# Optimization experiments

Hardware: AMD Instinct MI355X
Metric: run time of the kernel (lower is better)

## Reference

```python
import jax, jax.numpy as jnp
import numpy as np


def _fps(xyz, npoint):
    # Farthest point sampling. xyz: [B, N, 3] -> indices [B, npoint] (int32)
    B, N, _ = xyz.shape
    def step(carry, _):
        dist, far = carry
        centroid = jnp.take_along_axis(xyz, far[:, None, None], axis=1)  # [B,1,3]
        d = jnp.sum((xyz - centroid) ** 2, axis=-1)                      # [B,N]
        dist = jnp.minimum(dist, d)
        nxt = jnp.argmax(dist, axis=-1).astype(jnp.int32)
        return (dist, nxt), far
    init = (jnp.full((B, N), 1e10, xyz.dtype), jnp.zeros((B,), jnp.int32))
    _, inds = jax.lax.scan(step, init, None, length=npoint)
    return jnp.transpose(inds)  # [B, npoint]


def _gather(x, idx):
    # x: [B, N, C]; idx: [B, ...] -> [B, ..., C]
    return jax.vmap(lambda xb, ib: xb[ib])(x, idx)


def _knn(query, ref, k):
    # query: [B, M, 3]; ref: [B, N, 3] -> neighbor idx [B, M, k]
    d = (jnp.sum(query ** 2, -1, keepdims=True)
         - 2.0 * jnp.einsum('bmc,bnc->bmn', query, ref)
         + jnp.sum(ref ** 2, -1)[:, None, :])
    _, idx = jax.lax.top_k(-d, k)
    return idx


def _set_conv(xyz, feat, npoint, k, Ws, bs):
    # FPS downsample + KNN group + shared MLP + max-pool (FlowNet3D-style SetConv)
    fidx = _fps(xyz, npoint)
    new_xyz = _gather(xyz, fidx)                       # [B, npoint, 3]
    nidx = _knn(new_xyz, xyz, k)                       # [B, npoint, k]
    h = jnp.concatenate([_gather(xyz, nidx) - new_xyz[:, :, None, :],
                         _gather(feat, nidx)], axis=-1)
    for W, b in zip(Ws, bs):
        h = jax.nn.relu(h @ W + b)
    return jnp.max(h, axis=2), new_xyz, fidx


def _set_up_conv(cx, fx, cf, ff, k, Ws1, bs1, Ws2, bs2):
    # KNN from fine points into coarse set + MLP + max-pool + skip-concat + MLP
    nidx = _knn(fx, cx, k)                             # [B, M_fine, k]
    h = jnp.concatenate([_gather(cx, nidx) - fx[:, :, None, :],
                         _gather(cf, nidx)], axis=-1)
    for W, b in zip(Ws1, bs1):
        h = jax.nn.relu(h @ W + b)
    h = jnp.concatenate([jnp.max(h, axis=2), ff], axis=-1)
    for W, b in zip(Ws2, bs2):
        h = jax.nn.relu(h @ W + b)
    return h


def setup_inputs() -> dict:
    key = jax.random.key(0)
    ks = iter(jax.random.split(key, 64))
    def w(shape):
        return jax.random.normal(next(ks), shape, jnp.float32) / np.float32(np.sqrt(shape[0]))
    def z(n):
        return jnp.zeros((n,), jnp.float32)
    inp = {
        'pc': jax.random.normal(next(ks), (2, 8192, 3), jnp.float32),
        'feat': jax.random.normal(next(ks), (2, 8192, 3), jnp.float32),
        'd0_W': w((3, 32)), 'd0_b': z(32),
        'd1_W0': w((35, 32)), 'd1_b0': z(32), 'd1_W1': w((32, 64)), 'd1_b1': z(64),
        'd2_W0': w((67, 64)), 'd2_b0': z(64), 'd2_W1': w((64, 128)), 'd2_b1': z(128),
        'd3_W0': w((131, 128)), 'd3_b0': z(128), 'd3_W1': w((128, 192)), 'd3_b1': z(192),
        'd4_W0': w((195, 192)), 'd4_b0': z(192), 'd4_W1': w((192, 192)), 'd4_b1': z(192),
        'u4_W1': w((195, 192)), 'u4_b1': z(192), 'u4_W2': w((384, 192)), 'u4_b2': z(192),
        'u3_W1': w((195, 128)), 'u3_b1': z(128), 'u3_W2': w((256, 128)), 'u3_b2': z(128),
        'u2_W1': w((131, 64)), 'u2_b1': z(64), 'u2_W2': w((128, 64)), 'u2_b2': z(64),
        'u1_W1': w((67, 32)), 'u1_b1': z(32), 'u1_W2': w((64, 32)), 'u1_b2': z(32),
    }
    return inp


def reference(pc, feat,
              d0_W, d0_b,
              d1_W0, d1_b0, d1_W1, d1_b1,
              d2_W0, d2_b0, d2_W1, d2_b1,
              d3_W0, d3_b0, d3_W1, d3_b1,
              d4_W0, d4_b0, d4_W1, d4_b1,
              u4_W1, u4_b1, u4_W2, u4_b2,
              u3_W1, u3_b1, u3_W2, u3_b2,
              u2_W1, u2_b1, u2_W2, u2_b2,
              u1_W1, u1_b1, u1_W2, u1_b2):
    # gts[0] is None branch of GenFlow_unit_mask.forward: pure encoder pyramid.
    f0 = jax.nn.relu(feat @ d0_W + d0_b)                                   # down0 (1x1 Conv1d)
    f1, x1, i1 = _set_conv(pc, f0, 2048, 16, [d1_W0, d1_W1], [d1_b0, d1_b1])
    f2, x2, i2 = _set_conv(x1, f1, 512, 16, [d2_W0, d2_W1], [d2_b0, d2_b1])
    f3, x3, i3 = _set_conv(x2, f2, 128, 16, [d3_W0, d3_W1], [d3_b0, d3_b1])
    f4, x4, i4 = _set_conv(x3, f3, 64, 16, [d4_W0, d4_W1], [d4_b0, d4_b1])
    u3 = _set_up_conv(x4, x3, f4, f3, 8, [u4_W1], [u4_b1], [u4_W2], [u4_b2])
    u2 = _set_up_conv(x3, x2, u3, f2, 8, [u3_W1], [u3_b1], [u3_W2], [u3_b2])
    u1 = _set_up_conv(x2, x1, u2, f1, 8, [u2_W1], [u2_b1], [u2_W2], [u2_b2])
    u0 = _set_up_conv(x1, pc, u1, f0, 8, [u1_W1], [u1_b1], [u1_W2], [u1_b2])
    return (x1, x2, x3, i1, i2, i3, u0, u1, u2, u3)
```

## Files before the change

kernel.cpp:

```cpp
#include <hip/hip_runtime.h>
#include <cstdint>
#include <cstddef>


static __device__ __forceinline__ float sq3_rn(float x, float y, float z) {
    return __fadd_rn(__fadd_rn(__fmul_rn(x, x), __fmul_rn(y, y)), __fmul_rn(z, z));
}

static __device__ __forceinline__ unsigned int ford(float f) {
    unsigned int u = __float_as_uint(f);
    return u ^ ((u >> 31) ? 0xFFFFFFFFu : 0x80000000u);
}

template <int CTRL>
static __device__ __forceinline__ void dpp_max_step(unsigned& hi, unsigned& lo) {
    unsigned h2 = (unsigned)__builtin_amdgcn_update_dpp((int)hi, (int)hi, CTRL, 0xf, 0xf, false);
    unsigned l2 = (unsigned)__builtin_amdgcn_update_dpp((int)lo, (int)lo, CTRL, 0xf, 0xf, false);
    if (h2 > hi || (h2 == hi && l2 > lo)) { hi = h2; lo = l2; }
}
template <int CTRL>
static __device__ __forceinline__ void dpp_min_step(unsigned& hi, unsigned& lo) {
    unsigned h2 = (unsigned)__builtin_amdgcn_update_dpp((int)hi, (int)hi, CTRL, 0xf, 0xf, false);
    unsigned l2 = (unsigned)__builtin_amdgcn_update_dpp((int)lo, (int)lo, CTRL, 0xf, 0xf, false);
    if (h2 < hi || (h2 == hi && l2 < lo)) { hi = h2; lo = l2; }
}
static __device__ __forceinline__ void dpp_reduce_max_u64(unsigned& hi, unsigned& lo) {
    dpp_max_step<0x111>(hi, lo);
    dpp_max_step<0x112>(hi, lo);
    dpp_max_step<0x114>(hi, lo);
    dpp_max_step<0x118>(hi, lo);
    dpp_max_step<0x142>(hi, lo);
    dpp_max_step<0x143>(hi, lo);
}
static __device__ __forceinline__ void dpp_reduce_min_u64(unsigned& hi, unsigned& lo) {
    dpp_min_step<0x111>(hi, lo);
    dpp_min_step<0x112>(hi, lo);
    dpp_min_step<0x114>(hi, lo);
    dpp_min_step<0x118>(hi, lo);
    dpp_min_step<0x142>(hi, lo);
    dpp_min_step<0x143>(hi, lo);
}
static __device__ __forceinline__ void dpp_reduce_max_u64_4(unsigned& hi, unsigned& lo) {
    dpp_max_step<0x111>(hi, lo);
    dpp_max_step<0x112>(hi, lo);
}

template <int T, int P, bool MIRROR>
__global__ __launch_bounds__(T)
__attribute__((amdgpu_waves_per_eu(1, 1), amdgpu_num_vgpr(256)))
void fps_block(const float* __restrict__ xyz, int M,
               float* __restrict__ new_xyz, float* __restrict__ out_idx)
{
    constexpr int N = T * P;
    constexpr int NW = T / 64;
    static_assert(NW == 4, "slot scan hardcoded for 4 waves");
    const int b = blockIdx.x;
    const int t = threadIdx.x;
    const int lane = t & 63, wave = t >> 6;

    __shared__ unsigned long long s_slot[2][NW];
    __shared__ float spts[MIRROR ? N * 3 : 1];

    const float* x0 = xyz + (size_t)b * N * 3;
    if (MIRROR) {
        for (int i = t; i < N * 3; i += T) spts[i] = x0[i];
    }

    float px[P], py[P], pz[P], dist[P];
#pragma unroll
    for (int j = 0; j < P; ++j) {
        int p = j * T + t;
        px[j] = x0[p * 3 + 0];
        py[j] = x0[p * 3 + 1];
        pz[j] = x0[p * 3 + 2];
        dist[j] = 1e10f;
    }
    if (MIRROR) __syncthreads();

    int far = 0;
    for (int m = 0; m < M; ++m) {
        float cx, cy, cz;
        if (MIRROR) {
            cx = spts[far * 3 + 0];
            cy = spts[far * 3 + 1];
            cz = spts[far * 3 + 2];
        } else {
            cx = x0[far * 3 + 0];
            cy = x0[far * 3 + 1];
            cz = x0[far * 3 + 2];
        }
        if (t == 0) {
            size_t o = (size_t)b * M + m;
            new_xyz[o * 3 + 0] = cx;
            new_xyz[o * 3 + 1] = cy;
            new_xyz[o * 3 + 2] = cz;
            if (out_idx) out_idx[o] = (float)far;
        }
        float bv = -1.0f;
        int   bj = 0;
#pragma unroll
        for (int j = 0; j < P; ++j) {
            float dx = __fsub_rn(px[j], cx);
            float dy = __fsub_rn(py[j], cy);
            float dz = __fsub_rn(pz[j], cz);
            float d  = sq3_rn(dx, dy, dz);
            float nd = fminf(dist[j], d);
            dist[j] = nd;
            if (nd > bv) { bv = nd; bj = j; }
        }
        int bp = bj * T + t;
        unsigned hi = __float_as_uint(bv);
        unsigned lo = 0x7fffffffu - (unsigned)bp;
        dpp_reduce_max_u64(hi, lo);
        if (lane == 63)
            s_slot[m & 1][wave] = ((unsigned long long)hi << 32) | lo;
        __syncthreads();
        unsigned long long sv = s_slot[m & 1][lane & 3];
        unsigned shi = (unsigned)(sv >> 32), slo = (unsigned)(sv & 0xffffffffu);
        dpp_reduce_max_u64_4(shi, slo);
        unsigned wlo = (unsigned)__builtin_amdgcn_readlane((int)slo, 63);
        far = 0x7fffffff - (int)wlo;
    }
}

template <int P>
__global__ __launch_bounds__(64) __attribute__((amdgpu_waves_per_eu(1, 1)))
void fps_wave(const float* __restrict__ xyz, int M,
              float* __restrict__ new_xyz, float* __restrict__ out_idx)
{
    const int b = blockIdx.x;
    const int lane = threadIdx.x;
    const int N = 64 * P;
    const float* x0 = xyz + (size_t)b * N * 3;

    float px[P], py[P], pz[P], dist[P];
#pragma unroll
    for (int j = 0; j < P; ++j) {
        int p = j * 64 + lane;
        px[j] = x0[p * 3 + 0];
        py[j] = x0[p * 3 + 1];
        pz[j] = x0[p * 3 + 2];
        dist[j] = 1e10f;
    }

    int far = 0;
    for (int m = 0; m < M; ++m) {
        float cx = x0[far * 3 + 0];
        float cy = x0[far * 3 + 1];
        float cz = x0[far * 3 + 2];
        if (lane == 0) {
            size_t o = (size_t)b * M + m;
            new_xyz[o * 3 + 0] = cx;
            new_xyz[o * 3 + 1] = cy;
            new_xyz[o * 3 + 2] = cz;
            if (out_idx) out_idx[o] = (float)far;
        }
        float bv = -1.0f;
        int   bj = 0;
#pragma unroll
        for (int j = 0; j < P; ++j) {
            float dx = __fsub_rn(px[j], cx);
            float dy = __fsub_rn(py[j], cy);
            float dz = __fsub_rn(pz[j], cz);
            float d  = sq3_rn(dx, dy, dz);
            float nd = fminf(dist[j], d);
            dist[j] = nd;
            if (nd > bv) { bv = nd; bj = j; }
        }
        int bp = bj * 64 + lane;
        unsigned hi = __float_as_uint(bv);
        unsigned lo = 0x7fffffffu - (unsigned)bp;
        dpp_reduce_max_u64(hi, lo);
        unsigned wlo = (unsigned)__builtin_amdgcn_readlane((int)lo, 63);
        far = 0x7fffffff - (int)wlo;
    }
}

#define KNN_QPB 4
template <int K>
__global__ void knn_wave(const float* __restrict__ query, int M,
                         const float* __restrict__ ref, int N,
                         int* __restrict__ nidx)
{
    const int b = blockIdx.y;
    const int m = blockIdx.x * KNN_QPB + threadIdx.y;
    const int lane = threadIdx.x;
    if (m >= M) return;

    const float* qp = query + ((size_t)b * M + m) * 3;
    const float qx = qp[0], qy = qp[1], qz = qp[2];
    const float sq = sq3_rn(qx, qy, qz);

    float dk[K];
    int   ik[K];
#pragma unroll
    for (int j = 0; j < K; ++j) { dk[j] = INFINITY; ik[j] = 0x7fffffff; }

    const float* rb = ref + (size_t)b * N * 3;
    for (int n = lane; n < N; n += 64) {
        const float* rp = rb + (size_t)n * 3;
        float rx = rp[0], ry = rp[1], rz = rp[2];
        float sr = sq3_rn(rx, ry, rz);
        float dot = __fadd_rn(__fadd_rn(__fmul_rn(qx, rx), __fmul_rn(qy, ry)),
                              __fmul_rn(qz, rz));
        float d = __fadd_rn(__fsub_rn(sq, __fmul_rn(2.0f, dot)), sr);
        if (d < dk[K - 1]) {
            dk[K - 1] = d;
            ik[K - 1] = n;
#pragma unroll
            for (int j = K - 1; j > 0; --j) {
                if (dk[j] < dk[j - 1]) {
                    float tv = dk[j]; dk[j] = dk[j - 1]; dk[j - 1] = tv;
                    int   ti = ik[j]; ik[j] = ik[j - 1]; ik[j - 1] = ti;
                }
            }
        }
    }

    unsigned long long arr[K];
#pragma unroll
    for (int j = 0; j < K; ++j)
        arr[j] = ((unsigned long long)ford(dk[j]) << 32) | (unsigned int)ik[j];

    int winner = 0;
    for (int r = 0; r < K; ++r) {
        unsigned hi = (unsigned)(arr[0] >> 32);
        unsigned lo = (unsigned)(arr[0] & 0xffffffffu);
        dpp_reduce_min_u64(hi, lo);
        unsigned bhi = (unsigned)__builtin_amdgcn_readlane((int)hi, 63);
        unsigned blo = (unsigned)__builtin_amdgcn_readlane((int)lo, 63);
        unsigned long long best = ((unsigned long long)bhi << 32) | blo;
        if (lane == r) winner = (int)blo;
        if (arr[0] == best) {
#pragma unroll
            for (int j = 0; j < K - 1; ++j) arr[j] = arr[j + 1];
            arr[K - 1] = ~0ull;
        }
    }
    int* op = nidx + ((size_t)b * M + m) * K;
    if (lane < K) op[lane] = winner;
}

template <int K>
__global__ void setconv_kernel(const float* __restrict__ ref_xyz, int N,
                               const float* __restrict__ ref_feat, int Cin,
                               const float* __restrict__ new_xyz, int M,
                               const int* __restrict__ nidx,
                               const float* __restrict__ W0, const float* __restrict__ b0, int C1,
                               const float* __restrict__ W1, const float* __restrict__ b1, int C2,
                               float* __restrict__ out)
{
    const int b = blockIdx.y, q = blockIdx.x;
    const int lane = threadIdx.x;
    const int Cin3 = Cin + 3;
    extern __shared__ float sm[];
    float* h  = sm;
    float* h1 = sm + K * Cin3;

    const size_t qg = (size_t)b * M + q;
    const float cx = new_xyz[qg * 3 + 0];
    const float cy = new_xyz[qg * 3 + 1];
    const float cz = new_xyz[qg * 3 + 2];

    int nj[K];
#pragma unroll
    for (int j = 0; j < K; ++j) nj[j] = nidx[qg * K + j];

#pragma unroll
    for (int j = 0; j < K; ++j) {
        const float* xp = ref_xyz + ((size_t)b * N + nj[j]) * 3;
        const float* fp = ref_feat + ((size_t)b * N + nj[j]) * Cin;
        for (int i = lane; i < Cin3; i += 64) {
            float v;
            if (i == 0)      v = __fsub_rn(xp[0], cx);
            else if (i == 1) v = __fsub_rn(xp[1], cy);
            else if (i == 2) v = __fsub_rn(xp[2], cz);
            else             v = fp[i - 3];
            h[j * Cin3 + i] = v;
        }
    }
    __syncthreads();

    for (int c0 = 0; c0 < C1; c0 += 64) {
        int c = c0 + lane;
        bool act = c < C1;
        float acc[K];
        float bias = act ? b0[c] : 0.0f;
#pragma unroll
        for (int j = 0; j < K; ++j) acc[j] = bias;
        for (int i = 0; i < Cin3; ++i) {
            float w = act ? W0[(size_t)i * C1 + c] : 0.0f;
#pragma unroll
            for (int j = 0; j < K; ++j) acc[j] = fmaf(h[j * Cin3 + i], w, acc[j]);
        }
        if (act) {
#pragma unroll
            for (int j = 0; j < K; ++j) h1[j * C1 + c] = fmaxf(acc[j], 0.0f);
        }
    }
    __syncthreads();

    for (int c0 = 0; c0 < C2; c0 += 64) {
        int c = c0 + lane;
        bool act = c < C2;
        float acc[K];
        float bias = act ? b1[c] : 0.0f;
#pragma unroll
        for (int j = 0; j < K; ++j) acc[j] = bias;
        for (int i = 0; i < C1; ++i) {
            float w = act ? W1[(size_t)i * C2 + c] : 0.0f;
#pragma unroll
            for (int j = 0; j < K; ++j) acc[j] = fmaf(h1[j * C1 + i], w, acc[j]);
        }
        if (act) {
            float mv = acc[0];
#pragma unroll
            for (int j = 1; j < K; ++j) mv = fmaxf(mv, acc[j]);
            out[qg * C2 + c] = fmaxf(mv, 0.0f);
        }
    }
}

template <int K>
__global__ void setupconv_kernel(const float* __restrict__ cxyz, int Nc,
                                 const float* __restrict__ cf, int Cc,
                                 const float* __restrict__ fxyz, int M,
                                 const float* __restrict__ ff, int Cf,
                                 const int* __restrict__ nidx,
                                 const float* __restrict__ W1, const float* __restrict__ b1, int C1,
                                 const float* __restrict__ W2, const float* __restrict__ b2, int C2,
                                 float* __restrict__ out)
{
    const int b = blockIdx.y, q = blockIdx.x;
    const int lane = threadIdx.x;
    const int Cc3 = Cc + 3;
    extern __shared__ float sm[];
    float* h = sm;
    float* g = sm + K * Cc3;

    const size_t qg = (size_t)b * M + q;
    const float px = fxyz[qg * 3 + 0];
    const float py = fxyz[qg * 3 + 1];
    const float pz = fxyz[qg * 3 + 2];

    int nj[K];
#pragma unroll
    for (int j = 0; j < K; ++j) nj[j] = nidx[qg * K + j];

#pragma unroll
    for (int j = 0; j < K; ++j) {
        const float* xp = cxyz + ((size_t)b * Nc + nj[j]) * 3;
        const float* fp = cf + ((size_t)b * Nc + nj[j]) * Cc;
        for (int i = lane; i < Cc3; i += 64) {
            float v;
            if (i == 0)      v = __fsub_rn(xp[0], px);
            else if (i == 1) v = __fsub_rn(xp[1], py);
            else if (i == 2) v = __fsub_rn(xp[2], pz);
            else             v = fp[i - 3];
            h[j * Cc3 + i] = v;
        }
    }
    for (int i = lane; i < Cf; i += 64) g[C1 + i] = ff[qg * Cf + i];
    __syncthreads();

    for (int c0 = 0; c0 < C1; c0 += 64) {
        int c = c0 + lane;
        bool act = c < C1;
        float acc[K];
        float bias = act ? b1[c] : 0.0f;
#pragma unroll
        for (int j = 0; j < K; ++j) acc[j] = bias;
        for (int i = 0; i < Cc3; ++i) {
            float w = act ? W1[(size_t)i * C1 + c] : 0.0f;
#pragma unroll
            for (int j = 0; j < K; ++j) acc[j] = fmaf(h[j * Cc3 + i], w, acc[j]);
        }
        if (act) {
            float mv = acc[0];
#pragma unroll
            for (int j = 1; j < K; ++j) mv = fmaxf(mv, acc[j]);
            g[c] = fmaxf(mv, 0.0f);
        }
    }
    __syncthreads();

    const int Cg = C1 + Cf;
    for (int c0 = 0; c0 < C2; c0 += 64) {
        int c = c0 + lane;
        bool act = c < C2;
        float acc = act ? b2[c] : 0.0f;
        for (int i = 0; i < Cg; ++i) {
            float w = act ? W2[(size_t)i * C2 + c] : 0.0f;
            acc = fmaf(g[i], w, acc);
        }
        if (act) out[qg * C2 + c] = fmaxf(acc, 0.0f);
    }
}

__global__ void f0_kernel(const float* __restrict__ feat, const float* __restrict__ W,
                          const float* __restrict__ bias, float* __restrict__ out)
{
    int t = blockIdx.x * blockDim.x + threadIdx.x;
    int n = t >> 5, c = t & 31;
    const float* f = feat + (size_t)n * 3;
    float acc = bias[c];
    acc = fmaf(f[0], W[c], acc);
    acc = fmaf(f[1], W[32 + c], acc);
    acc = fmaf(f[2], W[64 + c], acc);
    out[t] = fmaxf(acc, 0.0f);
}


extern "C" void kernel_launch(void* const* d_in, const int* in_sizes, int n_in,
                              void* d_out, int out_size, void* d_ws, size_t ws_size,
                              hipStream_t stream)
{
    const float* pc    = (const float*)d_in[0];
    const float* feat  = (const float*)d_in[1];
    const float* d0_W  = (const float*)d_in[2];
    const float* d0_b  = (const float*)d_in[3];
    const float* d1_W0 = (const float*)d_in[4];
    const float* d1_b0 = (const float*)d_in[5];
    const float* d1_W1 = (const float*)d_in[6];
    const float* d1_b1 = (const float*)d_in[7];
    const float* d2_W0 = (const float*)d_in[8];
    const float* d2_b0 = (const float*)d_in[9];
    const float* d2_W1 = (const float*)d_in[10];
    const float* d2_b1 = (const float*)d_in[11];
    const float* d3_W0 = (const float*)d_in[12];
    const float* d3_b0 = (const float*)d_in[13];
    const float* d3_W1 = (const float*)d_in[14];
    const float* d3_b1 = (const float*)d_in[15];
    const float* d4_W0 = (const float*)d_in[16];
    const float* d4_b0 = (const float*)d_in[17];
    const float* d4_W1 = (const float*)d_in[18];
    const float* d4_b1 = (const float*)d_in[19];
    const float* u4_W1 = (const float*)d_in[20];
    const float* u4_b1 = (const float*)d_in[21];
    const float* u4_W2 = (const float*)d_in[22];
    const float* u4_b2 = (const float*)d_in[23];
    const float* u3_W1 = (const float*)d_in[24];
    const float* u3_b1 = (const float*)d_in[25];
    const float* u3_W2 = (const float*)d_in[26];
    const float* u3_b2 = (const float*)d_in[27];
    const float* u2_W1 = (const float*)d_in[28];
    const float* u2_b1 = (const float*)d_in[29];
    const float* u2_W2 = (const float*)d_in[30];
    const float* u2_b2 = (const float*)d_in[31];
    const float* u1_W1 = (const float*)d_in[32];
    const float* u1_b1 = (const float*)d_in[33];
    const float* u1_W2 = (const float*)d_in[34];
    const float* u1_b2 = (const float*)d_in[35];

    float* out = (float*)d_out;
    float* o_x1 = out + 0;
    float* o_x2 = out + 12288;
    float* o_x3 = out + 15360;
    float* o_i1 = out + 16128;
    float* o_i2 = out + 20224;
    float* o_i3 = out + 21248;
    float* o_u0 = out + 21504;
    float* o_u1 = out + 545792;
    float* o_u2 = out + 807936;
    float* o_u3 = out + 939008;

    float* w = (float*)d_ws;
    float* f0 = w; w += 2 * 8192 * 32;
    float* f1 = w; w += 2 * 2048 * 64;
    float* f2 = w; w += 2 * 512 * 128;
    float* f3 = w; w += 2 * 128 * 192;
    float* f4 = w; w += 2 * 64 * 192;
    float* x4 = w; w += 2 * 64 * 3;
    int* nidx = (int*)w;

    const int B = 2;
    const dim3 kb(64, KNN_QPB);

    f0_kernel<<<(2 * 8192 * 32) / 256, 256, 0, stream>>>(feat, d0_W, d0_b, f0);

    fps_block<256, 32, false><<<B, 256, 0, stream>>>(pc, 2048, o_x1, o_i1);
    knn_wave<16><<<dim3(2048 / KNN_QPB, B), kb, 0, stream>>>(o_x1, 2048, pc, 8192, nidx);
    setconv_kernel<16><<<dim3(2048, B), 64, (16 * 35 + 16 * 32) * 4, stream>>>(
        pc, 8192, f0, 32, o_x1, 2048, nidx, d1_W0, d1_b0, 32, d1_W1, d1_b1, 64, f1);

    fps_block<256, 8, true><<<B, 256, 0, stream>>>(o_x1, 512, o_x2, o_i2);
    knn_wave<16><<<dim3(512 / KNN_QPB, B), kb, 0, stream>>>(o_x2, 512, o_x1, 2048, nidx);
    setconv_kernel<16><<<dim3(512, B), 64, (16 * 67 + 16 * 64) * 4, stream>>>(
        o_x1, 2048, f1, 64, o_x2, 512, nidx, d2_W0, d2_b0, 64, d2_W1, d2_b1, 128, f2);

    fps_wave<8><<<B, 64, 0, stream>>>(o_x2, 128, o_x3, o_i3);
    knn_wave<16><<<dim3(128 / KNN_QPB, B), kb, 0, stream>>>(o_x3, 128, o_x2, 512, nidx);
    setconv_kernel<16><<<dim3(128, B), 64, (16 * 131 + 16 * 128) * 4, stream>>>(
        o_x2, 512, f2, 128, o_x3, 128, nidx, d3_W0, d3_b0, 128, d3_W1, d3_b1, 192, f3);

    fps_wave<2><<<B, 64, 0, stream>>>(o_x3, 64, x4, nullptr);
    knn_wave<16><<<dim3(64 / KNN_QPB, B), kb, 0, stream>>>(x4, 64, o_x3, 128, nidx);
    setconv_kernel<16><<<dim3(64, B), 64, (16 * 195 + 16 * 192) * 4, stream>>>(
        o_x3, 128, f3, 192, x4, 64, nidx, d4_W0, d4_b0, 192, d4_W1, d4_b1, 192, f4);

    knn_wave<8><<<dim3(128 / KNN_QPB, B), kb, 0, stream>>>(o_x3, 128, x4, 64, nidx);
    setupconv_kernel<8><<<dim3(128, B), 64, (8 * 195 + 192 + 192) * 4, stream>>>(
        x4, 64, f4, 192, o_x3, 128, f3, 192, nidx,
        u4_W1, u4_b1, 192, u4_W2, u4_b2, 192, o_u3);

    knn_wave<8><<<dim3(512 / KNN_QPB, B), kb, 0, stream>>>(o_x2, 512, o_x3, 128, nidx);
    setupconv_kernel<8><<<dim3(512, B), 64, (8 * 195 + 128 + 128) * 4, stream>>>(
        o_x3, 128, o_u3, 192, o_x2, 512, f2, 128, nidx,
        u3_W1, u3_b1, 128, u3_W2, u3_b2, 128, o_u2);

    knn_wave<8><<<dim3(2048 / KNN_QPB, B), kb, 0, stream>>>(o_x1, 2048, o_x2, 512, nidx);
    setupconv_kernel<8><<<dim3(2048, B), 64, (8 * 131 + 64 + 64) * 4, stream>>>(
        o_x2, 512, o_u2, 128, o_x1, 2048, f1, 64, nidx,
        u2_W1, u2_b1, 64, u2_W2, u2_b2, 64, o_u1);

    knn_wave<8><<<dim3(8192 / KNN_QPB, B), kb, 0, stream>>>(pc, 8192, o_x1, 2048, nidx);
    setupconv_kernel<8><<<dim3(8192, B), 64, (8 * 67 + 32 + 32) * 4, stream>>>(
        o_x1, 2048, o_u1, 64, pc, 8192, f0, 32, nidx,
        u1_W1, u1_b1, 32, u1_W2, u1_b2, 32, o_u0);
}
```

Before: 4.259 ms.

## Move FPS x/y coordinates to LDS and simplify cross-wave argmax

Farthest-point-sampling blocks now keep only z and running distances in registers, storing x/y pairs for all but the last slot in dynamically sized LDS. This cuts register pressure (the forced 256-VGPR attribute is dropped) at the cost of an LDS read per point on every iteration. The LDS point mirror is removed, so centroids are read from global memory each step. The cross-wave reduction is now a scalar loop over wave slots instead of a DPP reduction plus readlane.

```diff
diff --git a/kernel.cpp b/kernel.cpp
--- a/kernel.cpp
+++ b/kernel.cpp
@@ -40,55 +40,43 @@
     dpp_min_step<0x142>(hi, lo);
     dpp_min_step<0x143>(hi, lo);
 }
-static __device__ __forceinline__ void dpp_reduce_max_u64_4(unsigned& hi, unsigned& lo) {
-    dpp_max_step<0x111>(hi, lo);
-    dpp_max_step<0x112>(hi, lo);
-}
-
-template <int T, int P, bool MIRROR>
-__global__ __launch_bounds__(T)
-__attribute__((amdgpu_waves_per_eu(1, 1), amdgpu_num_vgpr(256)))
+
+template <int T, int P>
+__global__ __launch_bounds__(T) __attribute__((amdgpu_waves_per_eu(1, 1)))
 void fps_block(const float* __restrict__ xyz, int M,
                float* __restrict__ new_xyz, float* __restrict__ out_idx)
 {
     constexpr int N = T * P;
     constexpr int NW = T / 64;
-    static_assert(NW == 4, "slot scan hardcoded for 4 waves");
+    constexpr int NL = N - T;
+    extern __shared__ char smem[];
+    float2* sxy = (float2*)smem;
+    unsigned long long* s_slot = (unsigned long long*)(smem + (size_t)NL * 8);
+
     const int b = blockIdx.x;
     const int t = threadIdx.x;
     const int lane = t & 63, wave = t >> 6;
-
-    __shared__ unsigned long long s_slot[2][NW];
-    __shared__ float spts[MIRROR ? N * 3 : 1];
-
     const float* x0 = xyz + (size_t)b * N * 3;
-    if (MIRROR) {
-        for (int i = t; i < N * 3; i += T) spts[i] = x0[i];
-    }
-
-    float px[P], py[P], pz[P], dist[P];
+
+    float pz[P], dist[P];
+    float lx = 0.0f, ly = 0.0f;
 #pragma unroll
     for (int j = 0; j < P; ++j) {
         int p = j * T + t;
-        px[j] = x0[p * 3 + 0];
-        py[j] = x0[p * 3 + 1];
-        pz[j] = x0[p * 3 + 2];
+        float x = x0[p * 3 + 0];
+        float y = x0[p * 3 + 1];
+        pz[j]   = x0[p * 3 + 2];
         dist[j] = 1e10f;
-    }
-    if (MIRROR) __syncthreads();
+        if (j < P - 1) sxy[p] = make_float2(x, y);
+        else { lx = x; ly = y; }
+    }
+    __syncthreads();
 
     int far = 0;
     for (int m = 0; m < M; ++m) {
-        float cx, cy, cz;
-        if (MIRROR) {
-            cx = spts[far * 3 + 0];
-            cy = spts[far * 3 + 1];
-            cz = spts[far * 3 + 2];
-        } else {
-            cx = x0[far * 3 + 0];
-            cy = x0[far * 3 + 1];
-            cz = x0[far * 3 + 2];
-        }
+        float cx = x0[far * 3 + 0];
+        float cy = x0[far * 3 + 1];
+        float cz = x0[far * 3 + 2];
         if (t == 0) {
             size_t o = (size_t)b * M + m;
             new_xyz[o * 3 + 0] = cx;
@@ -100,8 +88,11 @@
         int   bj = 0;
 #pragma unroll
         for (int j = 0; j < P; ++j) {
-            float dx = __fsub_rn(px[j], cx);
-            float dy = __fsub_rn(py[j], cy);
+            float x, y;
+            if (j < P - 1) { float2 v = sxy[j * T + t]; x = v.x; y = v.y; }
+            else           { x = lx; y = ly; }
+            float dx = __fsub_rn(x, cx);
+            float dy = __fsub_rn(y, cy);
             float dz = __fsub_rn(pz[j], cz);
             float d  = sq3_rn(dx, dy, dz);
             float nd = fminf(dist[j], d);
@@ -113,13 +104,15 @@
         unsigned lo = 0x7fffffffu - (unsigned)bp;
         dpp_reduce_max_u64(hi, lo);
         if (lane == 63)
-            s_slot[m & 1][wave] = ((unsigned long long)hi << 32) | lo;
+            s_slot[(m & 1) * NW + wave] = ((unsigned long long)hi << 32) | lo;
         __syncthreads();
-        unsigned long long sv = s_slot[m & 1][lane & 3];
-        unsigned shi = (unsigned)(sv >> 32), slo = (unsigned)(sv & 0xffffffffu);
-        dpp_reduce_max_u64_4(shi, slo);
-        unsigned wlo = (unsigned)__builtin_amdgcn_readlane((int)slo, 63);
-        far = 0x7fffffff - (int)wlo;
+        unsigned long long best = s_slot[(m & 1) * NW];
+#pragma unroll
+        for (int w2 = 1; w2 < NW; ++w2) {
+            unsigned long long o = s_slot[(m & 1) * NW + w2];
+            if (o > best) best = o;
+        }
+        far = 0x7fffffff - (int)(unsigned int)(best & 0xffffffffu);
     }
 }
 
@@ -476,14 +469,17 @@
     const int B = 2;
     const dim3 kb(64, KNN_QPB);
 
+    const size_t fps1_lds = (size_t)(8192 - 256) * 8 + 2 * 4 * 8;
+    const size_t fps2_lds = (size_t)(2048 - 256) * 8 + 2 * 4 * 8;
+
     f0_kernel<<<(2 * 8192 * 32) / 256, 256, 0, stream>>>(feat, d0_W, d0_b, f0);
 
-    fps_block<256, 32, false><<<B, 256, 0, stream>>>(pc, 2048, o_x1, o_i1);
+    fps_block<256, 32><<<B, 256, fps1_lds, stream>>>(pc, 2048, o_x1, o_i1);
     knn_wave<16><<<dim3(2048 / KNN_QPB, B), kb, 0, stream>>>(o_x1, 2048, pc, 8192, nidx);
     setconv_kernel<16><<<dim3(2048, B), 64, (16 * 35 + 16 * 32) * 4, stream>>>(
         pc, 8192, f0, 32, o_x1, 2048, nidx, d1_W0, d1_b0, 32, d1_W1, d1_b1, 64, f1);
 
-    fps_block<256, 8, true><<<B, 256, 0, stream>>>(o_x1, 512, o_x2, o_i2);
+    fps_block<256, 8><<<B, 256, fps2_lds, stream>>>(o_x1, 512, o_x2, o_i2);
     knn_wave<16><<<dim3(512 / KNN_QPB, B), kb, 0, stream>>>(o_x2, 512, o_x1, 2048, nidx);
     setconv_kernel<16><<<dim3(512, B), 64, (16 * 67 + 16 * 64) * 4, stream>>>(
         o_x1, 2048, f1, 64, o_x2, 512, nidx, d2_W0, d2_b0, 64, d2_W1, d2_b1, 128, f2);
```

Result: slower. 4.845 ms (+13.8%).
